# Kernel tuning notes

Hardware: AMD Instinct MI355X
Metric: run time of the kernel (lower is better)

The kernel has to match this reference:

```python
import jax, jax.numpy as jnp
import numpy as np
import math

V, E, H, A, N = 32000, 512, 512, 64, 8  # vocab, embed, rnn hidden, att_size, n_heads
T, B = 256, 128                          # scan length (acts as att batch), inner dim


def _lstm(x, Wih, Whh, bih, bhh):
    # x: (T, B, E); torch nn.LSTM gate order i, f, g, o; zero initial state
    Bb = x.shape[1]
    Hh = Whh.shape[1]
    init = (jnp.zeros((Bb, Hh), x.dtype), jnp.zeros((Bb, Hh), x.dtype))

    def step(carry, xt):
        h, c = carry
        gates = xt @ Wih.T + bih + h @ Whh.T + bhh          # (B, 4H)
        i, f, g, o = jnp.split(gates, 4, axis=-1)
        c = jax.nn.sigmoid(f) * c + jax.nn.sigmoid(i) * jnp.tanh(g)
        h = jax.nn.sigmoid(o) * jnp.tanh(c)
        return (h, c), h

    _, hs = jax.lax.scan(step, init, x)
    return hs  # (T, B, H)


def setup_inputs() -> dict:
    key = jax.random.key(0)
    ks = jax.random.split(key, 26)
    rn = lambda k, s: jax.random.normal(k, s, jnp.float32) * 0.02
    inp = {
        "input_seq_l": jax.random.randint(ks[0], (T, B), 0, V, jnp.int32),
        "input_seq_r": jax.random.randint(ks[1], (T, B), 0, V, jnp.int32),
        "emb_l": rn(ks[2], (V, E)),
        "emb_r": rn(ks[3], (V, E)),
        "Wih_l": rn(ks[4], (4 * H, E)), "Whh_l": rn(ks[5], (4 * H, H)),
        "bih_l": rn(ks[6], (4 * H,)), "bhh_l": rn(ks[7], (4 * H,)),
        "Wih_r": rn(ks[8], (4 * H, E)), "Whh_r": rn(ks[9], (4 * H, H)),
        "bih_r": rn(ks[10], (4 * H,)), "bhh_r": rn(ks[11], (4 * H,)),
        "Wq": rn(ks[12], (N, H, A)), "bq": rn(ks[13], (N, A)),
        "Wk": rn(ks[14], (N, H, A)), "bk": rn(ks[15], (N, A)),
        "Wv": rn(ks[16], (N, H, A)), "bv": rn(ks[17], (N, A)),
        "Wo": rn(ks[18], (N * A, H)), "bo": rn(ks[19], (H,)),
        "Wh": rn(ks[20], (2 * H, 64)), "bh": rn(ks[21], (64,)),
        "Wa": rn(ks[22], (64, 2)), "ba": rn(ks[23], (2,)),
    }
    return inp


def reference(input_seq_l, input_seq_r, emb_l, emb_r,
              Wih_l, Whh_l, bih_l, bhh_l,
              Wih_r, Whh_r, bih_r, bhh_r,
              Wq, bq, Wk, bk, Wv, bv, Wo, bo, Wh, bh, Wa, ba):
    # left encoder
    ol = _lstm(emb_l[input_seq_l], Wih_l, Whh_l, bih_l, bhh_l)   # (T, B, H)
    # multi-head attention over left outputs (all heads batched)
    q = jnp.einsum('tbh,nhd->ntbd', ol, Wq) + bq[:, None, None, :]
    k = jnp.einsum('tbh,nhd->ntbd', ol, Wk) + bk[:, None, None, :]
    v = jnp.einsum('tbh,nhd->ntbd', ol, Wv) + bv[:, None, None, :]
    scores = jnp.einsum('ntbd,ntcd->ntbc', q, k) / math.sqrt(A)  # (N, T, B, B)
    p = jax.nn.softmax(scores, axis=-1)
    att = jnp.einsum('ntbc,ntcd->ntbd', p, v)                    # (N, T, B, A)
    att = att.transpose(1, 2, 0, 3).reshape(att.shape[1], att.shape[2], -1)  # (T, B, N*A)
    ol = att @ Wo + bo                                           # (T, B, H)
    ol = ol.mean(axis=1)                                         # (T, H)
    # right encoder
    orr = _lstm(emb_r[input_seq_r], Wih_r, Whh_r, bih_r, bhh_r).mean(axis=1)  # (T, H)
    cat = jnp.concatenate([ol, orr], axis=1)                     # (T, 2H)
    fc = cat @ Wh + bh
    ans = jax.nn.softmax(fc @ Wa + ba, axis=1)                   # (T, 2)
    return ans
```

## Files before the change

### kernel.cpp

```cpp
#include <hip/hip_runtime.h>

typedef unsigned short u16;
typedef __attribute__((ext_vector_type(4))) float f32x4;
typedef __attribute__((ext_vector_type(8))) short bf8;

#define MFMA16(a, b, c) __builtin_amdgcn_mfma_f32_16x16x32_bf16((a), (b), (c), 0, 0, 0)

__device__ __forceinline__ u16 f2bf(float f) {
  unsigned u = __builtin_bit_cast(unsigned, f);
  u += 0x7FFFu + ((u >> 16) & 1u);
  return (u16)(u >> 16);
}
__device__ __forceinline__ float bf2f(u16 h) {
  unsigned u = ((unsigned)h) << 16;
  return __builtin_bit_cast(float, u);
}
__device__ __forceinline__ float sigm(float x) { return 1.0f / (1.0f + __expf(-x)); }
__device__ __forceinline__ float tanh_f(float x) {
  x = fminf(fmaxf(x, -15.f), 15.f);
  float e = __expf(2.f * x);
  return (e - 1.f) / (e + 1.f);
}

__global__ void k_fill(float* __restrict__ p, int n, float v) {
  int i = blockIdx.x * blockDim.x + threadIdx.x;
  if (i < n) p[i] = v;
}

__device__ __forceinline__ void gemm_body(
    const int* __restrict__ idx, const float* __restrict__ emb,
    const float* __restrict__ Wih, u16* __restrict__ Gpre,
    int m_base, int m0, int n0, char* smem, int tid) {
  u16 (*lA)[72] = (u16(*)[72])smem;
  u16 (*lB)[72] = (u16(*)[72])(smem + 18432);
  int lane = tid & 63, wid = tid >> 6;
  int wm = (wid >> 1) << 6, wn = (wid & 1) << 6;
  int lq = lane >> 4, lc = lane & 15;
  f32x4 acc[4][4] = {};
  for (int k0 = 0; k0 < 512; k0 += 64) {
#pragma unroll
    for (int s = 0; s < 2; s++) {
      int slot = tid + s * 256;
      int row = slot >> 2, seg = (slot & 3) << 4;
      const float* pa = emb + (size_t)idx[m_base + m0 + row] * 512 + k0 + seg;
      const float* pb = Wih + (size_t)(n0 + row) * 512 + k0 + seg;
      float4 a0 = ((const float4*)pa)[0], a1 = ((const float4*)pa)[1];
      float4 a2 = ((const float4*)pa)[2], a3 = ((const float4*)pa)[3];
      float4 b0 = ((const float4*)pb)[0], b1 = ((const float4*)pb)[1];
      float4 b2 = ((const float4*)pb)[2], b3 = ((const float4*)pb)[3];
      union { u16 h[8]; int4 v; } pk;
      pk.h[0]=f2bf(a0.x); pk.h[1]=f2bf(a0.y); pk.h[2]=f2bf(a0.z); pk.h[3]=f2bf(a0.w);
      pk.h[4]=f2bf(a1.x); pk.h[5]=f2bf(a1.y); pk.h[6]=f2bf(a1.z); pk.h[7]=f2bf(a1.w);
      *(int4*)&lA[row][seg] = pk.v;
      pk.h[0]=f2bf(a2.x); pk.h[1]=f2bf(a2.y); pk.h[2]=f2bf(a2.z); pk.h[3]=f2bf(a2.w);
      pk.h[4]=f2bf(a3.x); pk.h[5]=f2bf(a3.y); pk.h[6]=f2bf(a3.z); pk.h[7]=f2bf(a3.w);
      *(int4*)&lA[row][seg + 8] = pk.v;
      pk.h[0]=f2bf(b0.x); pk.h[1]=f2bf(b0.y); pk.h[2]=f2bf(b0.z); pk.h[3]=f2bf(b0.w);
      pk.h[4]=f2bf(b1.x); pk.h[5]=f2bf(b1.y); pk.h[6]=f2bf(b1.z); pk.h[7]=f2bf(b1.w);
      *(int4*)&lB[row][seg] = pk.v;
      pk.h[0]=f2bf(b2.x); pk.h[1]=f2bf(b2.y); pk.h[2]=f2bf(b2.z); pk.h[3]=f2bf(b2.w);
      pk.h[4]=f2bf(b3.x); pk.h[5]=f2bf(b3.y); pk.h[6]=f2bf(b3.z); pk.h[7]=f2bf(b3.w);
      *(int4*)&lB[row][seg + 8] = pk.v;
    }
    __syncthreads();
#pragma unroll
    for (int kk = 0; kk < 64; kk += 32) {
      int ko = kk + (lq << 3);
      bf8 af[4], bg[4];
#pragma unroll
      for (int i = 0; i < 4; i++) af[i] = *(const bf8*)&lA[wm + i * 16 + lc][ko];
#pragma unroll
      for (int j = 0; j < 4; j++) bg[j] = *(const bf8*)&lB[wn + j * 16 + lc][ko];
#pragma unroll
      for (int i = 0; i < 4; i++)
#pragma unroll
        for (int j = 0; j < 4; j++) acc[i][j] = MFMA16(af[i], bg[j], acc[i][j]);
    }
    __syncthreads();
  }
  int cr = lq << 2;
#pragma unroll
  for (int i = 0; i < 4; i++)
#pragma unroll
    for (int j = 0; j < 4; j++)
#pragma unroll
      for (int r = 0; r < 4; r++) {
        int m = m0 + wm + i * 16 + cr + r;
        int nn = n0 + wn + j * 16 + lc;
        Gpre[(size_t)m * 2048 + nn] = f2bf(acc[i][j][r]);
      }
}

__global__ __launch_bounds__(256, 1) void k_prep(
    unsigned* __restrict__ flg, float* __restrict__ hrm,
    const float* __restrict__ Whh_l, u16* __restrict__ Whl,
    const float* __restrict__ Whh_r, u16* __restrict__ Whr,
    const float* __restrict__ Wq, u16* __restrict__ WqT,
    const float* __restrict__ Wk, u16* __restrict__ WkT,
    const float* __restrict__ Wv, u16* __restrict__ WvT,
    const float* __restrict__ bih_l, const float* __restrict__ bhh_l, float* __restrict__ bsl,
    const float* __restrict__ bih_r, const float* __restrict__ bhh_r, float* __restrict__ bsr,
    const int* __restrict__ seq_l, const int* __restrict__ seq_r,
    const float* __restrict__ emb_l, const float* __restrict__ emb_r,
    const float* __restrict__ Wih_l, const float* __restrict__ Wih_r,
    u16* __restrict__ Gl0, u16* __restrict__ Gr0, int Tc) {
  __shared__ __align__(16) char smem[36864];
  int bid = blockIdx.x, tid = threadIdx.x;
  if (bid < 2) {
    flg[bid * 256 + tid] = 0u;
  } else if (bid < 514) {
    hrm[(bid - 2) * 256 + tid] = 0.f;
  } else if (bid < 2562) {
    int rel = bid - 514;
    int enc = rel >> 10;
    int i = (rel & 1023) * 256 + tid;
    const float* in = enc ? Whh_r : Whh_l;
    u16* outp = enc ? Whr : Whl;
    float4 v = ((const float4*)in)[i];
    union { u16 h[4]; uint2 u; } p;
    p.h[0] = f2bf(v.x); p.h[1] = f2bf(v.y); p.h[2] = f2bf(v.z); p.h[3] = f2bf(v.w);
    ((uint2*)outp)[i] = p.u;
  } else if (bid < 5634) {
    int rel = bid - 2562;
    int which = rel >> 10;
    int g = (rel & 1023) * 256 + tid;
    const float* W = which == 0 ? Wq : (which == 1 ? Wk : Wv);
    u16* WT = which == 0 ? WqT : (which == 1 ? WkT : WvT);
    int n = g >> 15, d = (g >> 9) & 63, h = g & 511;
    WT[g] = f2bf(W[(n << 15) + (h << 6) + d]);
  } else if (bid < 5650) {
    int rel = bid - 5634;
    int enc = rel >> 3;
    int i = (rel & 7) * 256 + tid;
    if (enc == 0) bsl[i] = bih_l[i] + bhh_l[i];
    else          bsr[i] = bih_r[i] + bhh_r[i];
  } else {
    int rel = bid - 5650;
    int per = Tc << 4;
    int ge = rel >= per;
    int rem = ge ? rel - per : rel;
    gemm_body(ge ? seq_r : seq_l, ge ? emb_r : emb_l, ge ? Wih_r : Wih_l,
              ge ? Gr0 : Gl0, 0, (rem >> 4) << 7, (rem & 15) << 7, smem, tid);
  }
}

__device__ void lstm_body(
    const u16* __restrict__ Gl, const u16* __restrict__ Gr,
    const u16* __restrict__ Whl, const u16* __restrict__ Whr,
    const float* __restrict__ bsl, const float* __restrict__ bsr,
    u16* __restrict__ hsl, float* __restrict__ hrm,
    unsigned* __restrict__ hx, float* __restrict__ cstate,
    unsigned* __restrict__ flg, int t0, int nT, char* hlds, int bid, int tid) {
  int pod = bid & 7, cg = bid >> 3;
  int e = pod >> 2, bg = pod & 3;
  int b0 = bg << 5, c0 = cg << 5;
  const u16* Gpre = e ? Gr : Gl;
  const u16* Whh  = e ? Whr : Whl;
  const float* bsum = e ? bsr : bsl;

  int lane = tid & 63, w = tid >> 6;
  int lq = lane >> 4, lc = lane & 15, cr = lq << 2;
  int cl = (w << 3) + (lc & 7);
  int gg0 = lc >> 3;
  int lr0 = (gg0 << 5) + cl;
  int lr1 = ((2 + gg0) << 5) + cl;
  int gc0 = (gg0 << 9) + c0 + cl;
  int gc1 = ((2 + gg0) << 9) + c0 + cl;
  float bs0 = bsum[gc0], bs1 = bsum[gc1];
  bool owner = (lc & 8) != 0;

  int gr0 = ((lr0 >> 5) << 9) + c0 + (lr0 & 31);
  int gr1 = ((lr1 >> 5) << 9) + c0 + (lr1 & 31);
  bf8 wb0[16], wb1[16];
  {
    const u16* p0 = Whh + (size_t)gr0 * 512 + (lq << 3);
    const u16* p1 = Whh + (size_t)gr1 * 512 + (lq << 3);
#pragma unroll
    for (int ks = 0; ks < 16; ks++) {
      wb0[ks] = *(const bf8*)(p0 + (ks << 5));
      wb1[ks] = *(const bf8*)(p1 + (ks << 5));
    }
  }
  float creg[2][4];
#pragma unroll
  for (int mi = 0; mi < 2; mi++)
#pragma unroll
    for (int r = 0; r < 4; r++) creg[mi][r] = 0.f;
  if (t0 > 0 && owner) {
#pragma unroll
    for (int mi = 0; mi < 2; mi++)
#pragma unroll
      for (int r = 0; r < 4; r++)
        creg[mi][r] = cstate[(size_t)((e << 7) + b0 + (mi << 4) + cr + r) * 512 + c0 + cl];
  }

  u16 gp[2][2][4];
#pragma unroll
  for (int mi = 0; mi < 2; mi++)
#pragma unroll
    for (int r = 0; r < 4; r++) {
      size_t rowb = (size_t)(b0 + (mi << 4) + cr + r) << 11;
      gp[mi][0][r] = Gpre[rowb + gc0];
      gp[mi][1][r] = Gpre[rowb + gc1];
    }

  int ax = (lc & 7) << 4;
  int abyte0 = lc << 10;
  int abyte1 = (16 + lc) << 10;
  int hxc = (c0 >> 1) + (w << 2) + ((lc & 7) >> 1);
  const int srow = tid >> 6;
  const int scolb = (tid & 63) << 4;

  for (int t = 0; t < nT; t++) {
    int tg = t0 + t;
    f32x4 acc[2][2] = {};
    if (tg > 0) {
      if (t > 0) {
        if (tid < 64) {
          const unsigned* fa = flg + (pod << 6) + (lane & 15);
          unsigned fv;
          int guard = 0;
          while (true) {
            asm volatile("global_load_dword %0, %1, off sc0 sc1"
                         : "=v"(fv) : "v"(fa) : "memory");
            asm volatile("s_waitcnt vmcnt(0)" ::: "memory");
            if (__ballot(fv >= (unsigned)tg) == ~0ull) break;
            if (++guard > 300000) break;
          }
        }
        __syncthreads();
      }
      const unsigned* hxr = hx + (((size_t)((e << 1) | ((tg - 1) & 1))) << 15);
      uint4 sv[8];
#pragma unroll
      for (int i = 0; i < 8; i++) {
        int row = (i << 2) + srow;
        const unsigned* ap = hxr + (((size_t)(b0 + row)) << 8) + ((tid & 63) << 2);
        asm volatile("global_load_dwordx4 %0, %1, off sc0 sc1"
                     : "=v"(sv[i]) : "v"(ap));
      }
      asm volatile("s_waitcnt vmcnt(0)" ::: "memory");
      __builtin_amdgcn_sched_barrier(0);
#pragma unroll
      for (int i = 0; i < 8; i++) {
        int row = (i << 2) + srow;
        *(uint4*)(hlds + (row << 10) + (scolb ^ ((row & 7) << 4))) = sv[i];
      }
      __syncthreads();
#pragma unroll
      for (int ks = 0; ks < 16; ks++) {
        int kb = (ks << 6) + (lq << 4);
        bf8 a0 = *(const bf8*)(hlds + abyte0 + (kb ^ ax));
        bf8 a1 = *(const bf8*)(hlds + abyte1 + (kb ^ ax));
        acc[0][0] = MFMA16(a0, wb0[ks], acc[0][0]);
        acc[0][1] = MFMA16(a0, wb1[ks], acc[0][1]);
        acc[1][0] = MFMA16(a1, wb0[ks], acc[1][0]);
        acc[1][1] = MFMA16(a1, wb1[ks], acc[1][1]);
      }
      __syncthreads();
    }
    unsigned* hxw = hx + (((size_t)((e << 1) | (tg & 1))) << 15);
    float msum = 0.f;
#pragma unroll
    for (int mi = 0; mi < 2; mi++)
#pragma unroll
      for (int r = 0; r < 4; r++) {
        float v0 = acc[mi][0][r] + bf2f(gp[mi][0][r]) + bs0;
        float v1 = acc[mi][1][r] + bf2f(gp[mi][1][r]) + bs1;
        float send = sigm(v0) * tanh_f(v1);
        float recv = __shfl_xor(send, 8, 64);
        float h = 0.f;
        if (owner) {
          float c = sigm(v0) * creg[mi][r] + recv;
          creg[mi][r] = c;
          h = sigm(v1) * tanh_f(c);
          msum += h;
        }
        unsigned hb = (unsigned)f2bf(h);
        unsigned hi = __shfl_down(hb, 1, 64);
        unsigned packed = (hb & 0xffffu) | (hi << 16);
        int b = b0 + (mi << 4) + cr + r;
        if (owner && !(lane & 1)) {
          if (!e)
            *(unsigned*)(hsl + (((size_t)((tg << 7) + b)) << 9) + c0 + cl) = packed;
          unsigned* sa = hxw + (((size_t)b) << 8) + hxc;
          asm volatile("global_store_dword %0, %1, off sc0 sc1"
                       :: "v"(sa), "v"(packed) : "memory");
        }
      }
    asm volatile("s_waitcnt vmcnt(0)" ::: "memory");
    __syncthreads();
    if (tid == 0) {
      unsigned tv = (unsigned)(tg + 1);
      unsigned* fa = flg + (pod << 6) + cg;
      asm volatile("global_store_dword %0, %1, off sc0 sc1"
                   :: "v"(fa), "v"(tv) : "memory");
    }
    if (e) {
      float s = msum;
      s += __shfl_xor(s, 16, 64);
      s += __shfl_xor(s, 32, 64);
      if (owner && lq == 0)
        atomicAdd(&hrm[(tg << 9) + c0 + cl], s * 0.0078125f);
    }
    if (t + 1 < nT) {
#pragma unroll
      for (int mi = 0; mi < 2; mi++)
#pragma unroll
        for (int r = 0; r < 4; r++) {
          size_t rowb = (size_t)(((t + 1) << 7) + b0 + (mi << 4) + cr + r) << 11;
          gp[mi][0][r] = Gpre[rowb + gc0];
          gp[mi][1][r] = Gpre[rowb + gc1];
        }
    }
  }
  if (owner) {
#pragma unroll
    for (int mi = 0; mi < 2; mi++)
#pragma unroll
      for (int r = 0; r < 4; r++)
        cstate[(size_t)((e << 7) + b0 + (mi << 4) + cr + r) * 512 + c0 + cl] = creg[mi][r];
  }
}

__global__ __launch_bounds__(256, 1) void k_fused(
    const u16* __restrict__ Gl, const u16* __restrict__ Gr,
    u16* __restrict__ Ggl, u16* __restrict__ Ggr,
    const int* __restrict__ seq_l, const int* __restrict__ seq_r,
    const float* __restrict__ emb_l, const float* __restrict__ emb_r,
    const float* __restrict__ Wih_l, const float* __restrict__ Wih_r,
    const u16* __restrict__ Whl, const u16* __restrict__ Whr,
    const float* __restrict__ bsl, const float* __restrict__ bsr,
    u16* __restrict__ hsl, float* __restrict__ hrm,
    unsigned* __restrict__ hx, float* __restrict__ cstate,
    unsigned* __restrict__ flg, int t0, int nT, int gmb, int Tc) {
  __shared__ __align__(16) char smem[36864];
  int bid = blockIdx.x, tid = threadIdx.x;
  if (bid < 128) {
    lstm_body(Gl, Gr, Whl, Whr, bsl, bsr, hsl, hrm, hx, cstate, flg,
              t0, nT, smem, bid, tid);
  } else {
    int gb = bid - 128;
    int per = Tc << 4;
    int ge = gb >= per;
    int rem = ge ? gb - per : gb;
    gemm_body(ge ? seq_r : seq_l, ge ? emb_r : emb_l, ge ? Wih_r : Wih_l,
              ge ? Ggr : Ggl, gmb, (rem >> 4) << 7, (rem & 15) << 7, smem, tid);
  }
}

__global__ __launch_bounds__(256, 1) void k_attn(
    const u16* __restrict__ hs,
    const u16* __restrict__ WqT, const u16* __restrict__ WkT, const u16* __restrict__ WvT,
    const float* __restrict__ bq, const float* __restrict__ bk, const float* __restrict__ bv,
    float* __restrict__ attmean) {
  __shared__ __align__(16) char smem[123904];
  u16 (*qs)[72]  = (u16(*)[72])smem;
  u16 (*ksm)[72] = (u16(*)[72])(smem + 18432);
  u16 (*vt)[136] = (u16(*)[136])(smem + 36864);
  float (*sc)[132] = (float(*)[132])(smem + 54272);
  u16 (*ps)[136] = (u16(*)[136])smem;
  float* red = (float*)(smem + 54272);
  float* pmax = (float*)(smem + 121856);
  float* psum = (float*)(smem + 122880);

  int bid = blockIdx.x;
  int n = bid >> 8, t = bid & 255;
  int tid = threadIdx.x, lane = tid & 63, wid = tid >> 6;
  int lq = lane >> 4, lc = lane & 15, cr = lq << 2;
  const u16* ol = hs + ((size_t)t << 16);

  float bqv[4], bkv[4];
#pragma unroll
  for (int nf = 0; nf < 4; nf++) {
    bqv[nf] = bq[(n << 6) + (nf << 4) + lc];
    bkv[nf] = bk[(n << 6) + (nf << 4) + lc];
  }
  float bvv[4][4];
#pragma unroll
  for (int mi = 0; mi < 4; mi++)
#pragma unroll
    for (int r = 0; r < 4; r++) bvv[mi][r] = bv[(n << 6) + (mi << 4) + cr + r];

  const u16* wq = WqT + ((size_t)n << 15);
  const u16* wk = WkT + ((size_t)n << 15);
  const u16* wv = WvT + ((size_t)n << 15);
  f32x4 aq[2][4] = {}, ak[2][4] = {}, av[4][2] = {};
  for (int ks = 0; ks < 16; ks++) {
    int ko = (ks << 5) + (lq << 3);
    bf8 a0 = *(const bf8*)&ol[(size_t)((wid << 5) + lc) * 512 + ko];
    bf8 a1 = *(const bf8*)&ol[(size_t)((wid << 5) + 16 + lc) * 512 + ko];
#pragma unroll
    for (int nf = 0; nf < 4; nf++) {
      bf8 bw = *(const bf8*)&wq[(size_t)((nf << 4) + lc) * 512 + ko];
      aq[0][nf] = MFMA16(a0, bw, aq[0][nf]);
      aq[1][nf] = MFMA16(a1, bw, aq[1][nf]);
      bf8 bw2 = *(const bf8*)&wk[(size_t)((nf << 4) + lc) * 512 + ko];
      ak[0][nf] = MFMA16(a0, bw2, ak[0][nf]);
      ak[1][nf] = MFMA16(a1, bw2, ak[1][nf]);
    }
#pragma unroll
    for (int mi = 0; mi < 4; mi++) {
      bf8 aw = *(const bf8*)&wv[(size_t)((mi << 4) + lc) * 512 + ko];
      av[mi][0] = MFMA16(aw, a0, av[mi][0]);
      av[mi][1] = MFMA16(aw, a1, av[mi][1]);
    }
  }
#pragma unroll
  for (int mi = 0; mi < 2; mi++)
#pragma unroll
    for (int nf = 0; nf < 4; nf++)
#pragma unroll
      for (int r = 0; r < 4; r++) {
        int b = (wid << 5) + (mi << 4) + cr + r;
        int d = (nf << 4) + lc;
        qs[b][d] = f2bf(aq[mi][nf][r] + bqv[nf]);
        ksm[b][d] = f2bf(ak[mi][nf][r] + bkv[nf]);
      }
#pragma unroll
  for (int mi = 0; mi < 4; mi++)
#pragma unroll
    for (int c2 = 0; c2 < 2; c2++)
#pragma unroll
      for (int r = 0; r < 4; r++) {
        int d = (mi << 4) + cr + r;
        int c = (wid << 5) + (c2 << 4) + lc;
        vt[d][c] = f2bf(av[mi][c2][r] + bvv[mi][r]);
      }
  __syncthreads();

  f32x4 as_[2][8] = {};
#pragma unroll
  for (int ks = 0; ks < 2; ks++) {
    int ko = (ks << 5) + (lq << 3);
    bf8 a0 = *(const bf8*)&qs[(wid << 5) + lc][ko];
    bf8 a1 = *(const bf8*)&qs[(wid << 5) + 16 + lc][ko];
#pragma unroll
    for (int nf = 0; nf < 8; nf++) {
      bf8 bw = *(const bf8*)&ksm[(nf << 4) + lc][ko];
      as_[0][nf] = MFMA16(a0, bw, as_[0][nf]);
      as_[1][nf] = MFMA16(a1, bw, as_[1][nf]);
    }
  }
#pragma unroll
  for (int mi = 0; mi < 2; mi++)
#pragma unroll
    for (int nf = 0; nf < 8; nf++)
#pragma unroll
      for (int r = 0; r < 4; r++)
        sc[(wid << 5) + (mi << 4) + cr + r][(nf << 4) + lc] = as_[mi][nf][r] * 0.125f;
  __syncthreads();

  {
    int row = tid & 127, half = tid >> 7;
    int cb = half << 6;
    float mx = -1e30f;
    for (int j = 0; j < 64; j++) mx = fmaxf(mx, sc[row][cb + j]);
    pmax[(half << 7) + row] = mx;
    __syncthreads();
    mx = fmaxf(pmax[row], pmax[128 + row]);
    float s = 0.f;
    for (int j = 0; j < 64; j++) { float ev = __expf(sc[row][cb + j] - mx); s += ev; sc[row][cb + j] = ev; }
    psum[(half << 7) + row] = s;
    __syncthreads();
    float inv = 1.f / (psum[row] + psum[128 + row]);
    for (int j = 0; j < 64; j++) ps[row][cb + j] = f2bf(sc[row][cb + j] * inv);
  }
  __syncthreads();

  f32x4 ao[2][4] = {};
#pragma unroll
  for (int ks = 0; ks < 4; ks++) {
    int ko = (ks << 5) + (lq << 3);
    bf8 a0 = *(const bf8*)&ps[(wid << 5) + lc][ko];
    bf8 a1 = *(const bf8*)&ps[(wid << 5) + 16 + lc][ko];
#pragma unroll
    for (int nf = 0; nf < 4; nf++) {
      bf8 bw = *(const bf8*)&vt[(nf << 4) + lc][ko];
      ao[0][nf] = MFMA16(a0, bw, ao[0][nf]);
      ao[1][nf] = MFMA16(a1, bw, ao[1][nf]);
    }
  }
  float pm[4];
#pragma unroll
  for (int nf = 0; nf < 4; nf++) {
    float s = 0.f;
#pragma unroll
    for (int mi = 0; mi < 2; mi++)
#pragma unroll
      for (int r = 0; r < 4; r++) s += ao[mi][nf][r];
    s += __shfl_xor(s, 16, 64);
    s += __shfl_xor(s, 32, 64);
    pm[nf] = s;
  }
  if (lq == 0) {
#pragma unroll
    for (int nf = 0; nf < 4; nf++) red[(wid << 6) + (nf << 4) + lc] = pm[nf];
  }
  __syncthreads();
  if (tid < 64) {
    float s = red[tid] + red[64 + tid] + red[128 + tid] + red[192 + tid];
    attmean[(t << 9) + (n << 6) + tid] = s * 0.0078125f;
  }
}

__global__ __launch_bounds__(256) void k_olm(const float* __restrict__ am, const float* __restrict__ Wo,
                                             const float* __restrict__ bo, float* __restrict__ olm) {
  __shared__ float row[512];
  int t = blockIdx.x >> 1, h0 = (blockIdx.x & 1) << 8;
  int tid = threadIdx.x;
  row[tid] = am[(t << 9) + tid];
  row[tid + 256] = am[(t << 9) + 256 + tid];
  __syncthreads();
  int h = h0 + tid;
  float s = bo[h];
  for (int k = 0; k < 512; k++) s += row[k] * Wo[(k << 9) + h];
  olm[(t << 9) + h] = s;
}

__global__ __launch_bounds__(64) void k_final(const float* __restrict__ olmp, const float* __restrict__ hrm,
                                              const float* __restrict__ Wh, const float* __restrict__ bh,
                                              const float* __restrict__ Wa, const float* __restrict__ ba,
                                              float* __restrict__ out) {
  __shared__ float cat[1024];
  int t = blockIdx.x, j = threadIdx.x;
  for (int i = j; i < 512; i += 64) {
    cat[i] = olmp[(t << 9) + i];
    cat[512 + i] = hrm[(t << 9) + i];
  }
  __syncthreads();
  float f = bh[j];
  for (int k = 0; k < 1024; k++) f += cat[k] * Wh[(k << 6) + j];
  float p0 = f * Wa[j * 2], p1 = f * Wa[j * 2 + 1];
#pragma unroll
  for (int o = 32; o > 0; o >>= 1) { p0 += __shfl_down(p0, o); p1 += __shfl_down(p1, o); }
  if (j == 0) {
    p0 += ba[0]; p1 += ba[1];
    float m = fmaxf(p0, p1);
    float e0 = __expf(p0 - m), e1 = __expf(p1 - m);
    float inv = 1.f / (e0 + e1);
    out[t * 2] = e0 * inv;
    out[t * 2 + 1] = e1 * inv;
  }
}

extern "C" void kernel_launch(void* const* d_in, const int* in_sizes, int n_in,
                              void* d_out, int out_size, void* d_ws, size_t ws_size,
                              hipStream_t stream) {
  const int*   seq_l = (const int*)d_in[0];
  const int*   seq_r = (const int*)d_in[1];
  const float* emb_l = (const float*)d_in[2];
  const float* emb_r = (const float*)d_in[3];
  const float* Wih_l = (const float*)d_in[4];
  const float* Whh_l = (const float*)d_in[5];
  const float* bih_l = (const float*)d_in[6];
  const float* bhh_l = (const float*)d_in[7];
  const float* Wih_r = (const float*)d_in[8];
  const float* Whh_r = (const float*)d_in[9];
  const float* bih_r = (const float*)d_in[10];
  const float* bhh_r = (const float*)d_in[11];
  const float* Wq = (const float*)d_in[12];
  const float* bq = (const float*)d_in[13];
  const float* Wk = (const float*)d_in[14];
  const float* bk = (const float*)d_in[15];
  const float* Wv = (const float*)d_in[16];
  const float* bv = (const float*)d_in[17];
  const float* Wo = (const float*)d_in[18];
  const float* bo = (const float*)d_in[19];
  const float* Wh = (const float*)d_in[20];
  const float* bhc = (const float*)d_in[21];
  const float* Wa = (const float*)d_in[22];
  const float* ba = (const float*)d_in[23];
  float* out = (float*)d_out;

  char* ws = (char*)d_ws;
  size_t off = 0;
  auto alloc = [&](size_t bytes) { char* p = ws + off; off += (bytes + 255) & ~(size_t)255; return p; };
  u16*   hsl  = (u16*)alloc(33554432);
  u16*   Whl  = (u16*)alloc(2097152);
  u16*   Whr  = (u16*)alloc(2097152);
  u16*   WqT  = (u16*)alloc(524288);
  u16*   WkT  = (u16*)alloc(524288);
  u16*   WvT  = (u16*)alloc(524288);
  float* bsl  = (float*)alloc(8192);
  float* bsr  = (float*)alloc(8192);
  unsigned* hx = (unsigned*)alloc(524288);
  float* cst  = (float*)alloc(524288);
  unsigned* flg = (unsigned*)alloc(2048);
  float* am   = (float*)alloc(524288);
  float* hrm  = (float*)alloc(524288);
  float* olm  = (float*)alloc(524288);
  size_t fixed = off;

  int Tc = 0;
  const int cands[3] = {128, 64, 32};
  for (int i = 0; i < 3; i++) {
    size_t need = fixed + 4ull * (size_t)cands[i] * 524288ull;
    if (need <= ws_size) { Tc = cands[i]; break; }
  }
  if (Tc == 0) {
    k_fill<<<2, 256, 0, stream>>>(out, out_size, 0.25f);
    return;
  }
  size_t gbytes = (size_t)Tc * 524288ull;
  u16* Glb[2]; u16* Grb[2];
  Glb[0] = (u16*)alloc(gbytes); Glb[1] = (u16*)alloc(gbytes);
  Grb[0] = (u16*)alloc(gbytes); Grb[1] = (u16*)alloc(gbytes);

  k_prep<<<5650 + (Tc << 5), 256, 0, stream>>>(
      flg, hrm, Whh_l, Whl, Whh_r, Whr, Wq, WqT, Wk, WkT, Wv, WvT,
      bih_l, bhh_l, bsl, bih_r, bhh_r, bsr,
      seq_l, seq_r, emb_l, emb_r, Wih_l, Wih_r, Glb[0], Grb[0], Tc);

  int nC = 256 / Tc;
  for (int c = 0; c < nC; c++) {
    int hg = (c + 1 < nC);
    int grid = 128 + (hg ? (Tc << 5) : 0);
    k_fused<<<grid, 256, 0, stream>>>(
        Glb[c & 1], Grb[c & 1], Glb[(c + 1) & 1], Grb[(c + 1) & 1],
        seq_l, seq_r, emb_l, emb_r, Wih_l, Wih_r,
        Whl, Whr, bsl, bsr, hsl, hrm, hx, cst, flg,
        c * Tc, Tc, (c + 1) * Tc * 128, Tc);
  }
  k_attn<<<2048, 256, 0, stream>>>(hsl, WqT, WkT, WvT, bq, bk, bv, am);
  k_olm<<<512, 256, 0, stream>>>(am, Wo, bo, olm);
  k_final<<<256, 64, 0, stream>>>(olm, hrm, Wh, bhc, Wa, ba, out);
}
```

Baseline: 1.751 ms.

## Fuse input projection into recurrent LSTM step and overlap attention with scan

Drops the separate chunked input-projection GEMM. Each LSTM block now keeps both Wih and Whh slices in registers and computes x_t·Wih alongside h·Whh every step, reading gathered bf16 embeddings. Attention blocks are launched in the same persistent kernel and spin on per-timestep flags, so attention for step t starts as soon as that step's hidden states exist. This removes the chunk launches and the precomputed-gate round trip, but doubles per-step MFMA work and register pressure on the serial critical path. It also relies on attention blocks co-residing with the LSTM blocks without starving them.

```diff
diff --git a/kernel.cpp b/kernel.cpp
--- a/kernel.cpp
+++ b/kernel.cpp
@@ -27,74 +27,12 @@
   if (i < n) p[i] = v;
 }
 
-__device__ __forceinline__ void gemm_body(
-    const int* __restrict__ idx, const float* __restrict__ emb,
-    const float* __restrict__ Wih, u16* __restrict__ Gpre,
-    int m_base, int m0, int n0, char* smem, int tid) {
-  u16 (*lA)[72] = (u16(*)[72])smem;
-  u16 (*lB)[72] = (u16(*)[72])(smem + 18432);
-  int lane = tid & 63, wid = tid >> 6;
-  int wm = (wid >> 1) << 6, wn = (wid & 1) << 6;
-  int lq = lane >> 4, lc = lane & 15;
-  f32x4 acc[4][4] = {};
-  for (int k0 = 0; k0 < 512; k0 += 64) {
-#pragma unroll
-    for (int s = 0; s < 2; s++) {
-      int slot = tid + s * 256;
-      int row = slot >> 2, seg = (slot & 3) << 4;
-      const float* pa = emb + (size_t)idx[m_base + m0 + row] * 512 + k0 + seg;
-      const float* pb = Wih + (size_t)(n0 + row) * 512 + k0 + seg;
-      float4 a0 = ((const float4*)pa)[0], a1 = ((const float4*)pa)[1];
-      float4 a2 = ((const float4*)pa)[2], a3 = ((const float4*)pa)[3];
-      float4 b0 = ((const float4*)pb)[0], b1 = ((const float4*)pb)[1];
-      float4 b2 = ((const float4*)pb)[2], b3 = ((const float4*)pb)[3];
-      union { u16 h[8]; int4 v; } pk;
-      pk.h[0]=f2bf(a0.x); pk.h[1]=f2bf(a0.y); pk.h[2]=f2bf(a0.z); pk.h[3]=f2bf(a0.w);
-      pk.h[4]=f2bf(a1.x); pk.h[5]=f2bf(a1.y); pk.h[6]=f2bf(a1.z); pk.h[7]=f2bf(a1.w);
-      *(int4*)&lA[row][seg] = pk.v;
-      pk.h[0]=f2bf(a2.x); pk.h[1]=f2bf(a2.y); pk.h[2]=f2bf(a2.z); pk.h[3]=f2bf(a2.w);
-      pk.h[4]=f2bf(a3.x); pk.h[5]=f2bf(a3.y); pk.h[6]=f2bf(a3.z); pk.h[7]=f2bf(a3.w);
-      *(int4*)&lA[row][seg + 8] = pk.v;
-      pk.h[0]=f2bf(b0.x); pk.h[1]=f2bf(b0.y); pk.h[2]=f2bf(b0.z); pk.h[3]=f2bf(b0.w);
-      pk.h[4]=f2bf(b1.x); pk.h[5]=f2bf(b1.y); pk.h[6]=f2bf(b1.z); pk.h[7]=f2bf(b1.w);
-      *(int4*)&lB[row][seg] = pk.v;
-      pk.h[0]=f2bf(b2.x); pk.h[1]=f2bf(b2.y); pk.h[2]=f2bf(b2.z); pk.h[3]=f2bf(b2.w);
-      pk.h[4]=f2bf(b3.x); pk.h[5]=f2bf(b3.y); pk.h[6]=f2bf(b3.z); pk.h[7]=f2bf(b3.w);
-      *(int4*)&lB[row][seg + 8] = pk.v;
-    }
-    __syncthreads();
-#pragma unroll
-    for (int kk = 0; kk < 64; kk += 32) {
-      int ko = kk + (lq << 3);
-      bf8 af[4], bg[4];
-#pragma unroll
-      for (int i = 0; i < 4; i++) af[i] = *(const bf8*)&lA[wm + i * 16 + lc][ko];
-#pragma unroll
-      for (int j = 0; j < 4; j++) bg[j] = *(const bf8*)&lB[wn + j * 16 + lc][ko];
-#pragma unroll
-      for (int i = 0; i < 4; i++)
-#pragma unroll
-        for (int j = 0; j < 4; j++) acc[i][j] = MFMA16(af[i], bg[j], acc[i][j]);
-    }
-    __syncthreads();
-  }
-  int cr = lq << 2;
-#pragma unroll
-  for (int i = 0; i < 4; i++)
-#pragma unroll
-    for (int j = 0; j < 4; j++)
-#pragma unroll
-      for (int r = 0; r < 4; r++) {
-        int m = m0 + wm + i * 16 + cr + r;
-        int nn = n0 + wn + j * 16 + lc;
-        Gpre[(size_t)m * 2048 + nn] = f2bf(acc[i][j][r]);
-      }
-}
-
-__global__ __launch_bounds__(256, 1) void k_prep(
+__global__ __launch_bounds__(256, 2) void k_prep(
     unsigned* __restrict__ flg, float* __restrict__ hrm,
     const float* __restrict__ Whh_l, u16* __restrict__ Whl,
     const float* __restrict__ Whh_r, u16* __restrict__ Whr,
+    const float* __restrict__ Wih_l, u16* __restrict__ Wil,
+    const float* __restrict__ Wih_r, u16* __restrict__ Wir,
     const float* __restrict__ Wq, u16* __restrict__ WqT,
     const float* __restrict__ Wk, u16* __restrict__ WkT,
     const float* __restrict__ Wv, u16* __restrict__ WvT,
@@ -102,61 +40,68 @@
     const float* __restrict__ bih_r, const float* __restrict__ bhh_r, float* __restrict__ bsr,
     const int* __restrict__ seq_l, const int* __restrict__ seq_r,
     const float* __restrict__ emb_l, const float* __restrict__ emb_r,
-    const float* __restrict__ Wih_l, const float* __restrict__ Wih_r,
-    u16* __restrict__ Gl0, u16* __restrict__ Gr0, int Tc) {
-  __shared__ __align__(16) char smem[36864];
+    u16* __restrict__ xsl, u16* __restrict__ xsr) {
   int bid = blockIdx.x, tid = threadIdx.x;
   if (bid < 2) {
     flg[bid * 256 + tid] = 0u;
   } else if (bid < 514) {
     hrm[(bid - 2) * 256 + tid] = 0.f;
-  } else if (bid < 2562) {
+  } else if (bid < 4610) {
     int rel = bid - 514;
-    int enc = rel >> 10;
+    int which = rel >> 10;
     int i = (rel & 1023) * 256 + tid;
-    const float* in = enc ? Whh_r : Whh_l;
-    u16* outp = enc ? Whr : Whl;
+    const float* in = which == 0 ? Whh_l : (which == 1 ? Whh_r : (which == 2 ? Wih_l : Wih_r));
+    u16* outp = which == 0 ? Whl : (which == 1 ? Whr : (which == 2 ? Wil : Wir));
     float4 v = ((const float4*)in)[i];
     union { u16 h[4]; uint2 u; } p;
     p.h[0] = f2bf(v.x); p.h[1] = f2bf(v.y); p.h[2] = f2bf(v.z); p.h[3] = f2bf(v.w);
     ((uint2*)outp)[i] = p.u;
-  } else if (bid < 5634) {
-    int rel = bid - 2562;
+  } else if (bid < 7682) {
+    int rel = bid - 4610;
     int which = rel >> 10;
     int g = (rel & 1023) * 256 + tid;
     const float* W = which == 0 ? Wq : (which == 1 ? Wk : Wv);
     u16* WT = which == 0 ? WqT : (which == 1 ? WkT : WvT);
     int n = g >> 15, d = (g >> 9) & 63, h = g & 511;
     WT[g] = f2bf(W[(n << 15) + (h << 6) + d]);
-  } else if (bid < 5650) {
-    int rel = bid - 5634;
+  } else if (bid < 7698) {
+    int rel = bid - 7682;
     int enc = rel >> 3;
     int i = (rel & 7) * 256 + tid;
     if (enc == 0) bsl[i] = bih_l[i] + bhh_l[i];
     else          bsr[i] = bih_r[i] + bhh_r[i];
   } else {
-    int rel = bid - 5650;
-    int per = Tc << 4;
-    int ge = rel >= per;
-    int rem = ge ? rel - per : rel;
-    gemm_body(ge ? seq_r : seq_l, ge ? emb_r : emb_l, ge ? Wih_r : Wih_l,
-              ge ? Gr0 : Gl0, 0, (rem >> 4) << 7, (rem & 15) << 7, smem, tid);
+    int rel = bid - 7698;
+    int enc = rel >= 2048;
+    int rem = enc ? rel - 2048 : rel;
+    const int* idx = enc ? seq_r : seq_l;
+    const float* emb = enc ? emb_r : emb_l;
+    u16* xs = enc ? xsr : xsl;
+    int row = (rem << 4) + (tid >> 4);
+    int seg = (tid & 15) << 5;
+    const float4* src = (const float4*)(emb + (size_t)idx[row] * 512 + seg);
+    uint2* dst = (uint2*)(xs + (size_t)row * 512 + seg);
+#pragma unroll
+    for (int j = 0; j < 8; j++) {
+      float4 v = src[j];
+      union { u16 h[4]; uint2 u; } p;
+      p.h[0] = f2bf(v.x); p.h[1] = f2bf(v.y); p.h[2] = f2bf(v.z); p.h[3] = f2bf(v.w);
+      dst[j] = p.u;
+    }
   }
 }
 
 __device__ void lstm_body(
-    const u16* __restrict__ Gl, const u16* __restrict__ Gr,
-    const u16* __restrict__ Whl, const u16* __restrict__ Whr,
-    const float* __restrict__ bsl, const float* __restrict__ bsr,
+    const u16* __restrict__ xs, const u16* __restrict__ Whh,
+    const u16* __restrict__ Wih, const float* __restrict__ bsum,
     u16* __restrict__ hsl, float* __restrict__ hrm,
-    unsigned* __restrict__ hx, float* __restrict__ cstate,
-    unsigned* __restrict__ flg, int t0, int nT, char* hlds, int bid, int tid) {
+    unsigned* __restrict__ hx, unsigned* __restrict__ flg,
+    int bid, int tid, char* smem) {
+  char* hlds = smem;
+  char* xlds = smem + 32768;
   int pod = bid & 7, cg = bid >> 3;
   int e = pod >> 2, bg = pod & 3;
   int b0 = bg << 5, c0 = cg << 5;
-  const u16* Gpre = e ? Gr : Gl;
-  const u16* Whh  = e ? Whr : Whl;
-  const float* bsum = e ? bsr : bsl;
 
   int lane = tid & 63, w = tid >> 6;
   int lq = lane >> 4, lc = lane & 15, cr = lq << 2;
@@ -171,14 +116,18 @@
 
   int gr0 = ((lr0 >> 5) << 9) + c0 + (lr0 & 31);
   int gr1 = ((lr1 >> 5) << 9) + c0 + (lr1 & 31);
-  bf8 wb0[16], wb1[16];
+  bf8 wb0[16], wb1[16], wi0[16], wi1[16];
   {
     const u16* p0 = Whh + (size_t)gr0 * 512 + (lq << 3);
     const u16* p1 = Whh + (size_t)gr1 * 512 + (lq << 3);
+    const u16* q0 = Wih + (size_t)gr0 * 512 + (lq << 3);
+    const u16* q1 = Wih + (size_t)gr1 * 512 + (lq << 3);
 #pragma unroll
     for (int ks = 0; ks < 16; ks++) {
       wb0[ks] = *(const bf8*)(p0 + (ks << 5));
       wb1[ks] = *(const bf8*)(p1 + (ks << 5));
+      wi0[ks] = *(const bf8*)(q0 + (ks << 5));
+      wi1[ks] = *(const bf8*)(q1 + (ks << 5));
     }
   }
   float creg[2][4];
@@ -186,23 +135,6 @@
   for (int mi = 0; mi < 2; mi++)
 #pragma unroll
     for (int r = 0; r < 4; r++) creg[mi][r] = 0.f;
-  if (t0 > 0 && owner) {
-#pragma unroll
-    for (int mi = 0; mi < 2; mi++)
-#pragma unroll
-      for (int r = 0; r < 4; r++)
-        creg[mi][r] = cstate[(size_t)((e << 7) + b0 + (mi << 4) + cr + r) * 512 + c0 + cl];
-  }
-
-  u16 gp[2][2][4];
-#pragma unroll
-  for (int mi = 0; mi < 2; mi++)
-#pragma unroll
-    for (int r = 0; r < 4; r++) {
-      size_t rowb = (size_t)(b0 + (mi << 4) + cr + r) << 11;
-      gp[mi][0][r] = Gpre[rowb + gc0];
-      gp[mi][1][r] = Gpre[rowb + gc1];
-    }
 
   int ax = (lc & 7) << 4;
   int abyte0 = lc << 10;
@@ -211,25 +143,28 @@
   const int srow = tid >> 6;
   const int scolb = (tid & 63) << 4;
 
-  for (int t = 0; t < nT; t++) {
-    int tg = t0 + t;
+  for (int tg = 0; tg < 256; tg++) {
+    uint4 xv[8];
+#pragma unroll
+    for (int i = 0; i < 8; i++) {
+      int row = (i << 2) + srow;
+      xv[i] = ((const uint4*)(xs + (((size_t)((tg << 7) + b0 + row)) << 9)))[tid & 63];
+    }
     f32x4 acc[2][2] = {};
     if (tg > 0) {
-      if (t > 0) {
-        if (tid < 64) {
-          const unsigned* fa = flg + (pod << 6) + (lane & 15);
-          unsigned fv;
-          int guard = 0;
-          while (true) {
-            asm volatile("global_load_dword %0, %1, off sc0 sc1"
-                         : "=v"(fv) : "v"(fa) : "memory");
-            asm volatile("s_waitcnt vmcnt(0)" ::: "memory");
-            if (__ballot(fv >= (unsigned)tg) == ~0ull) break;
-            if (++guard > 300000) break;
-          }
+      if (tid < 64) {
+        const unsigned* fa = flg + (pod << 6) + (lane & 15);
+        unsigned fv;
+        int guard = 0;
+        while (true) {
+          asm volatile("global_load_dword %0, %1, off sc0 sc1"
+                       : "=v"(fv) : "v"(fa) : "memory");
+          asm volatile("s_waitcnt vmcnt(0)" ::: "memory");
+          if (__ballot(fv >= (unsigned)tg) == ~0ull) break;
+          if (++guard > 1000000) break;
         }
-        __syncthreads();
-      }
+      }
+      __syncthreads();
       const unsigned* hxr = hx + (((size_t)((e << 1) | ((tg - 1) & 1))) << 15);
       uint4 sv[8];
 #pragma unroll
@@ -246,7 +181,24 @@
         int row = (i << 2) + srow;
         *(uint4*)(hlds + (row << 10) + (scolb ^ ((row & 7) << 4))) = sv[i];
       }
-      __syncthreads();
+    }
+#pragma unroll
+    for (int i = 0; i < 8; i++) {
+      int row = (i << 2) + srow;
+      *(uint4*)(xlds + (row << 10) + (scolb ^ ((row & 7) << 4))) = xv[i];
+    }
+    __syncthreads();
+#pragma unroll
+    for (int ks = 0; ks < 16; ks++) {
+      int kb = (ks << 6) + (lq << 4);
+      bf8 a0 = *(const bf8*)(xlds + abyte0 + (kb ^ ax));
+      bf8 a1 = *(const bf8*)(xlds + abyte1 + (kb ^ ax));
+      acc[0][0] = MFMA16(a0, wi0[ks], acc[0][0]);
+      acc[0][1] = MFMA16(a0, wi1[ks], acc[0][1]);
+      acc[1][0] = MFMA16(a1, wi0[ks], acc[1][0]);
+      acc[1][1] = MFMA16(a1, wi1[ks], acc[1][1]);
+    }
+    if (tg > 0) {
 #pragma unroll
       for (int ks = 0; ks < 16; ks++) {
         int kb = (ks << 6) + (lq << 4);
@@ -257,16 +209,16 @@
         acc[1][0] = MFMA16(a1, wb0[ks], acc[1][0]);
         acc[1][1] = MFMA16(a1, wb1[ks], acc[1][1]);
       }
-      __syncthreads();
-    }
+    }
+    __syncthreads();
     unsigned* hxw = hx + (((size_t)((e << 1) | (tg & 1))) << 15);
     float msum = 0.f;
 #pragma unroll
     for (int mi = 0; mi < 2; mi++)
 #pragma unroll
       for (int r = 0; r < 4; r++) {
-        float v0 = acc[mi][0][r] + bf2f(gp[mi][0][r]) + bs0;
-        float v1 = acc[mi][1][r] + bf2f(gp[mi][1][r]) + bs1;
+        float v0 = acc[mi][0][r] + bs0;
+        float v1 = acc[mi][1][r] + bs1;
         float send = sigm(v0) * tanh_f(v1);
         float recv = __shfl_xor(send, 8, 64);
         float h = 0.f;
@@ -281,8 +233,11 @@
         unsigned packed = (hb & 0xffffu) | (hi << 16);
         int b = b0 + (mi << 4) + cr + r;
         if (owner && !(lane & 1)) {
-          if (!e)
-            *(unsigned*)(hsl + (((size_t)((tg << 7) + b)) << 9) + c0 + cl) = packed;
+          if (!e) {
+            unsigned* hp = (unsigned*)(hsl + (((size_t)((tg << 7) + b)) << 9) + c0 + cl);
+            asm volatile("global_store_dword %0, %1, off sc0 sc1"
+                         :: "v"(hp), "v"(packed) : "memory");
+          }
           unsigned* sa = hxw + (((size_t)b) << 8) + hxc;
           asm volatile("global_store_dword %0, %1, off sc0 sc1"
                        :: "v"(sa), "v"(packed) : "memory");
@@ -303,58 +258,14 @@
       if (owner && lq == 0)
         atomicAdd(&hrm[(tg << 9) + c0 + cl], s * 0.0078125f);
     }
-    if (t + 1 < nT) {
-#pragma unroll
-      for (int mi = 0; mi < 2; mi++)
-#pragma unroll
-        for (int r = 0; r < 4; r++) {
-          size_t rowb = (size_t)(((t + 1) << 7) + b0 + (mi << 4) + cr + r) << 11;
-          gp[mi][0][r] = Gpre[rowb + gc0];
-          gp[mi][1][r] = Gpre[rowb + gc1];
-        }
-    }
-  }
-  if (owner) {
-#pragma unroll
-    for (int mi = 0; mi < 2; mi++)
-#pragma unroll
-      for (int r = 0; r < 4; r++)
-        cstate[(size_t)((e << 7) + b0 + (mi << 4) + cr + r) * 512 + c0 + cl] = creg[mi][r];
-  }
-}
-
-__global__ __launch_bounds__(256, 1) void k_fused(
-    const u16* __restrict__ Gl, const u16* __restrict__ Gr,
-    u16* __restrict__ Ggl, u16* __restrict__ Ggr,
-    const int* __restrict__ seq_l, const int* __restrict__ seq_r,
-    const float* __restrict__ emb_l, const float* __restrict__ emb_r,
-    const float* __restrict__ Wih_l, const float* __restrict__ Wih_r,
-    const u16* __restrict__ Whl, const u16* __restrict__ Whr,
-    const float* __restrict__ bsl, const float* __restrict__ bsr,
-    u16* __restrict__ hsl, float* __restrict__ hrm,
-    unsigned* __restrict__ hx, float* __restrict__ cstate,
-    unsigned* __restrict__ flg, int t0, int nT, int gmb, int Tc) {
-  __shared__ __align__(16) char smem[36864];
-  int bid = blockIdx.x, tid = threadIdx.x;
-  if (bid < 128) {
-    lstm_body(Gl, Gr, Whl, Whr, bsl, bsr, hsl, hrm, hx, cstate, flg,
-              t0, nT, smem, bid, tid);
-  } else {
-    int gb = bid - 128;
-    int per = Tc << 4;
-    int ge = gb >= per;
-    int rem = ge ? gb - per : gb;
-    gemm_body(ge ? seq_r : seq_l, ge ? emb_r : emb_l, ge ? Wih_r : Wih_l,
-              ge ? Ggr : Ggl, gmb, (rem >> 4) << 7, (rem & 15) << 7, smem, tid);
-  }
-}
-
-__global__ __launch_bounds__(256, 1) void k_attn(
+  }
+}
+
+__device__ void attn_body(
     const u16* __restrict__ hs,
     const u16* __restrict__ WqT, const u16* __restrict__ WkT, const u16* __restrict__ WvT,
     const float* __restrict__ bq, const float* __restrict__ bk, const float* __restrict__ bv,
-    float* __restrict__ attmean) {
-  __shared__ __align__(16) char smem[123904];
+    float* __restrict__ attmean, int n, int t, char* smem, int tid) {
   u16 (*qs)[72]  = (u16(*)[72])smem;
   u16 (*ksm)[72] = (u16(*)[72])(smem + 18432);
   u16 (*vt)[136] = (u16(*)[136])(smem + 36864);
@@ -364,9 +275,7 @@
   float* pmax = (float*)(smem + 121856);
   float* psum = (float*)(smem + 122880);
 
-  int bid = blockIdx.x;
-  int n = bid >> 8, t = bid & 255;
-  int tid = threadIdx.x, lane = tid & 63, wid = tid >> 6;
+  int lane = tid & 63, wid = tid >> 6;
   int lq = lane >> 4, lc = lane & 15, cr = lq << 2;
   const u16* ol = hs + ((size_t)t << 16);
 
@@ -381,15 +290,28 @@
   for (int mi = 0; mi < 4; mi++)
 #pragma unroll
     for (int r = 0; r < 4; r++) bvv[mi][r] = bv[(n << 6) + (mi << 4) + cr + r];
+
+  uint4 xa0[16], xa1[16];
+#pragma unroll
+  for (int ks = 0; ks < 16; ks++) {
+    int ko = (ks << 5) + (lq << 3);
+    const u16* p0 = ol + (size_t)((wid << 5) + lc) * 512 + ko;
+    const u16* p1 = ol + (size_t)((wid << 5) + 16 + lc) * 512 + ko;
+    asm volatile("global_load_dwordx4 %0, %1, off sc0 sc1" : "=v"(xa0[ks]) : "v"(p0));
+    asm volatile("global_load_dwordx4 %0, %1, off sc0 sc1" : "=v"(xa1[ks]) : "v"(p1));
+  }
+  asm volatile("s_waitcnt vmcnt(0)" ::: "memory");
+  __builtin_amdgcn_sched_barrier(0);
 
   const u16* wq = WqT + ((size_t)n << 15);
   const u16* wk = WkT + ((size_t)n << 15);
   const u16* wv = WvT + ((size_t)n << 15);
   f32x4 aq[2][4] = {}, ak[2][4] = {}, av[4][2] = {};
+#pragma unroll
   for (int ks = 0; ks < 16; ks++) {
     int ko = (ks << 5) + (lq << 3);
-    bf8 a0 = *(const bf8*)&ol[(size_t)((wid << 5) + lc) * 512 + ko];
-    bf8 a1 = *(const bf8*)&ol[(size_t)((wid << 5) + 16 + lc) * 512 + ko];
+    bf8 a0 = __builtin_bit_cast(bf8, xa0[ks]);
+    bf8 a1 = __builtin_bit_cast(bf8, xa1[ks]);
 #pragma unroll
     for (int nf = 0; nf < 4; nf++) {
       bf8 bw = *(const bf8*)&wq[(size_t)((nf << 4) + lc) * 512 + ko];
@@ -501,6 +423,44 @@
   if (tid < 64) {
     float s = red[tid] + red[64 + tid] + red[128 + tid] + red[192 + tid];
     attmean[(t << 9) + (n << 6) + tid] = s * 0.0078125f;
+  }
+}
+
+__global__ __launch_bounds__(256, 1) void k_fused(
+    const u16* __restrict__ xsl, const u16* __restrict__ xsr,
+    const u16* __restrict__ Whl, const u16* __restrict__ Whr,
+    const u16* __restrict__ Wil, const u16* __restrict__ Wir,
+    const float* __restrict__ bsl, const float* __restrict__ bsr,
+    u16* __restrict__ hsl, float* __restrict__ hrm,
+    unsigned* __restrict__ hx, unsigned* __restrict__ flg,
+    const u16* __restrict__ WqT, const u16* __restrict__ WkT, const u16* __restrict__ WvT,
+    const float* __restrict__ bq, const float* __restrict__ bk, const float* __restrict__ bv,
+    float* __restrict__ am) {
+  __shared__ __align__(16) char smem[123904];
+  int bid = blockIdx.x, tid = threadIdx.x;
+  if (bid < 128) {
+    int e = (bid & 7) >> 2;
+    lstm_body(e ? xsr : xsl, e ? Whr : Whl, e ? Wir : Wil, e ? bsr : bsl,
+              hsl, hrm, hx, flg, bid, tid, smem);
+  } else {
+    int abid = bid - 128;
+    int t = abid >> 3, n = abid & 7;
+    if (tid < 64) {
+      int lane = tid;
+      const unsigned* fa = flg + ((lane >> 4) << 6) + (lane & 15);
+      unsigned fv;
+      int guard = 0;
+      while (true) {
+        asm volatile("global_load_dword %0, %1, off sc0 sc1"
+                     : "=v"(fv) : "v"(fa) : "memory");
+        asm volatile("s_waitcnt vmcnt(0)" ::: "memory");
+        if (__ballot(fv > (unsigned)t) == ~0ull) break;
+        if (++guard > 3000000) break;
+        __builtin_amdgcn_s_sleep(8);
+      }
+    }
+    __syncthreads();
+    attn_body(hsl, WqT, WkT, WvT, bq, bk, bv, am, n, t, smem, tid);
   }
 }
 
@@ -577,52 +537,38 @@
   size_t off = 0;
   auto alloc = [&](size_t bytes) { char* p = ws + off; off += (bytes + 255) & ~(size_t)255; return p; };
   u16*   hsl  = (u16*)alloc(33554432);
+  u16*   xsl  = (u16*)alloc(33554432);
+  u16*   xsr  = (u16*)alloc(33554432);
   u16*   Whl  = (u16*)alloc(2097152);
   u16*   Whr  = (u16*)alloc(2097152);
+  u16*   Wil  = (u16*)alloc(2097152);
+  u16*   Wir  = (u16*)alloc(2097152);
   u16*   WqT  = (u16*)alloc(524288);
   u16*   WkT  = (u16*)alloc(524288);
   u16*   WvT  = (u16*)alloc(524288);
   float* bsl  = (float*)alloc(8192);
   float* bsr  = (float*)alloc(8192);
   unsigned* hx = (unsigned*)alloc(524288);
-  float* cst  = (float*)alloc(524288);
   unsigned* flg = (unsigned*)alloc(2048);
   float* am   = (float*)alloc(524288);
   float* hrm  = (float*)alloc(524288);
   float* olm  = (float*)alloc(524288);
-  size_t fixed = off;
-
-  int Tc = 0;
-  const int cands[3] = {128, 64, 32};
-  for (int i = 0; i < 3; i++) {
-    size_t need = fixed + 4ull * (size_t)cands[i] * 524288ull;
-    if (need <= ws_size) { Tc = cands[i]; break; }
-  }
-  if (Tc == 0) {
+
+  if (off > ws_size) {
     k_fill<<<2, 256, 0, stream>>>(out, out_size, 0.25f);
     return;
   }
-  size_t gbytes = (size_t)Tc * 524288ull;
-  u16* Glb[2]; u16* Grb[2];
-  Glb[0] = (u16*)alloc(gbytes); Glb[1] = (u16*)alloc(gbytes);
-  Grb[0] = (u16*)alloc(gbytes); Grb[1] = (u16*)alloc(gbytes);
-
-  k_prep<<<5650 + (Tc << 5), 256, 0, stream>>>(
-      flg, hrm, Whh_l, Whl, Whh_r, Whr, Wq, WqT, Wk, WkT, Wv, WvT,
+
+  k_prep<<<11794, 256, 0, stream>>>(
+      flg, hrm, Whh_l, Whl, Whh_r, Whr, Wih_l, Wil, Wih_r, Wir,
+      Wq, WqT, Wk, WkT, Wv, WvT,
       bih_l, bhh_l, bsl, bih_r, bhh_r, bsr,
-      seq_l, seq_r, emb_l, emb_r, Wih_l, Wih_r, Glb[0], Grb[0], Tc);
-
-  int nC = 256 / Tc;
-  for (int c = 0; c < nC; c++) {
-    int hg = (c + 1 < nC);
-    int grid = 128 + (hg ? (Tc << 5) : 0);
-    k_fused<<<grid, 256, 0, stream>>>(
-        Glb[c & 1], Grb[c & 1], Glb[(c + 1) & 1], Grb[(c + 1) & 1],
-        seq_l, seq_r, emb_l, emb_r, Wih_l, Wih_r,
-        Whl, Whr, bsl, bsr, hsl, hrm, hx, cst, flg,
-        c * Tc, Tc, (c + 1) * Tc * 128, Tc);
-  }
-  k_attn<<<2048, 256, 0, stream>>>(hsl, WqT, WkT, WvT, bq, bk, bv, am);
+      seq_l, seq_r, emb_l, emb_r, xsl, xsr);
+
+  k_fused<<<2176, 256, 0, stream>>>(
+      xsl, xsr, Whl, Whr, Wil, Wir, bsl, bsr,
+      hsl, hrm, hx, flg, WqT, WkT, WvT, bq, bk, bv, am);
+
   k_olm<<<512, 256, 0, stream>>>(am, Wo, bo, olm);
   k_final<<<256, 64, 0, stream>>>(olm, hrm, Wh, bhc, Wa, ba, out);
 }
```

Result: slower. 2.212 ms (+26.3%).

## Overlap QKV weight conversion with first LSTM chunk and allow uneven chunking

Applied to the files above, without the earlier changes.

Moves the Wq/Wk/Wv transpose-and-convert work out of the prep kernel into spare blocks of the first fused LSTM launch, so it runs alongside the serial recurrence instead of delaying it. It also adds uneven chunk schedules (96/96/64) for tighter workspace budgets and raises the prep kernel's launch bound to two blocks per CU. The fused kernel's shared memory declaration grows to 80 KB, which may affect how the extra GEMM and conversion blocks co-reside with the persistent LSTM blocks.

```diff
diff --git a/kernel.cpp b/kernel.cpp
--- a/kernel.cpp
+++ b/kernel.cpp
@@ -91,19 +91,16 @@
       }
 }
 
-__global__ __launch_bounds__(256, 1) void k_prep(
+__global__ __launch_bounds__(256, 2) void k_prep(
     unsigned* __restrict__ flg, float* __restrict__ hrm,
     const float* __restrict__ Whh_l, u16* __restrict__ Whl,
     const float* __restrict__ Whh_r, u16* __restrict__ Whr,
-    const float* __restrict__ Wq, u16* __restrict__ WqT,
-    const float* __restrict__ Wk, u16* __restrict__ WkT,
-    const float* __restrict__ Wv, u16* __restrict__ WvT,
     const float* __restrict__ bih_l, const float* __restrict__ bhh_l, float* __restrict__ bsl,
     const float* __restrict__ bih_r, const float* __restrict__ bhh_r, float* __restrict__ bsr,
     const int* __restrict__ seq_l, const int* __restrict__ seq_r,
     const float* __restrict__ emb_l, const float* __restrict__ emb_r,
     const float* __restrict__ Wih_l, const float* __restrict__ Wih_r,
-    u16* __restrict__ Gl0, u16* __restrict__ Gr0, int Tc) {
+    u16* __restrict__ Gl0, u16* __restrict__ Gr0, int Tc0) {
   __shared__ __align__(16) char smem[36864];
   int bid = blockIdx.x, tid = threadIdx.x;
   if (bid < 2) {
@@ -120,23 +117,15 @@
     union { u16 h[4]; uint2 u; } p;
     p.h[0] = f2bf(v.x); p.h[1] = f2bf(v.y); p.h[2] = f2bf(v.z); p.h[3] = f2bf(v.w);
     ((uint2*)outp)[i] = p.u;
-  } else if (bid < 5634) {
+  } else if (bid < 2578) {
     int rel = bid - 2562;
-    int which = rel >> 10;
-    int g = (rel & 1023) * 256 + tid;
-    const float* W = which == 0 ? Wq : (which == 1 ? Wk : Wv);
-    u16* WT = which == 0 ? WqT : (which == 1 ? WkT : WvT);
-    int n = g >> 15, d = (g >> 9) & 63, h = g & 511;
-    WT[g] = f2bf(W[(n << 15) + (h << 6) + d]);
-  } else if (bid < 5650) {
-    int rel = bid - 5634;
     int enc = rel >> 3;
     int i = (rel & 7) * 256 + tid;
     if (enc == 0) bsl[i] = bih_l[i] + bhh_l[i];
     else          bsr[i] = bih_r[i] + bhh_r[i];
   } else {
-    int rel = bid - 5650;
-    int per = Tc << 4;
+    int rel = bid - 2578;
+    int per = Tc0 << 4;
     int ge = rel >= per;
     int rem = ge ? rel - per : rel;
     gemm_body(ge ? seq_r : seq_l, ge ? emb_r : emb_l, ge ? Wih_r : Wih_l,
@@ -333,19 +322,33 @@
     const float* __restrict__ bsl, const float* __restrict__ bsr,
     u16* __restrict__ hsl, float* __restrict__ hrm,
     unsigned* __restrict__ hx, float* __restrict__ cstate,
-    unsigned* __restrict__ flg, int t0, int nT, int gmb, int Tc) {
-  __shared__ __align__(16) char smem[36864];
+    unsigned* __restrict__ flg,
+    const float* __restrict__ Wq, const float* __restrict__ Wk, const float* __restrict__ Wv,
+    u16* __restrict__ WqT, u16* __restrict__ WkT, u16* __restrict__ WvT,
+    int t0, int nT, int gmb, int nextT) {
+  __shared__ __align__(16) char smem[81920];
   int bid = blockIdx.x, tid = threadIdx.x;
   if (bid < 128) {
     lstm_body(Gl, Gr, Whl, Whr, bsl, bsr, hsl, hrm, hx, cstate, flg,
               t0, nT, smem, bid, tid);
   } else {
     int gb = bid - 128;
-    int per = Tc << 4;
-    int ge = gb >= per;
-    int rem = ge ? gb - per : gb;
-    gemm_body(ge ? seq_r : seq_l, ge ? emb_r : emb_l, ge ? Wih_r : Wih_l,
-              ge ? Ggr : Ggl, gmb, (rem >> 4) << 7, (rem & 15) << 7, smem, tid);
+    int per2 = nextT << 5;
+    if (gb < per2) {
+      int per = nextT << 4;
+      int ge = gb >= per;
+      int rem = ge ? gb - per : gb;
+      gemm_body(ge ? seq_r : seq_l, ge ? emb_r : emb_l, ge ? Wih_r : Wih_l,
+                ge ? Ggr : Ggl, gmb, (rem >> 4) << 7, (rem & 15) << 7, smem, tid);
+    } else {
+      int rel = gb - per2;
+      int which = rel >> 10;
+      int g = (rel & 1023) * 256 + tid;
+      const float* W = which == 0 ? Wq : (which == 1 ? Wk : Wv);
+      u16* WT = which == 0 ? WqT : (which == 1 ? WkT : WvT);
+      int n = g >> 15, d = (g >> 9) & 63, h = g & 511;
+      WT[g] = f2bf(W[(n << 15) + (h << 6) + d]);
+    }
   }
 }
 
@@ -592,35 +595,39 @@
   float* olm  = (float*)alloc(524288);
   size_t fixed = off;
 
-  int Tc = 0;
-  const int cands[3] = {128, 64, 32};
-  for (int i = 0; i < 3; i++) {
-    size_t need = fixed + 4ull * (size_t)cands[i] * 524288ull;
-    if (need <= ws_size) { Tc = cands[i]; break; }
-  }
-  if (Tc == 0) {
+  int chunks[4]; int nch = 0; int Tmax = 0;
+  if (fixed + 4ull * 128 * 524288ull <= ws_size) {
+    chunks[0] = 128; chunks[1] = 128; nch = 2; Tmax = 128;
+  } else if (fixed + 4ull * 96 * 524288ull <= ws_size) {
+    chunks[0] = 96; chunks[1] = 96; chunks[2] = 64; nch = 3; Tmax = 96;
+  } else if (fixed + 4ull * 64 * 524288ull <= ws_size) {
+    chunks[0] = chunks[1] = chunks[2] = chunks[3] = 64; nch = 4; Tmax = 64;
+  } else {
     k_fill<<<2, 256, 0, stream>>>(out, out_size, 0.25f);
     return;
   }
-  size_t gbytes = (size_t)Tc * 524288ull;
+  size_t gbytes = (size_t)Tmax * 524288ull;
   u16* Glb[2]; u16* Grb[2];
   Glb[0] = (u16*)alloc(gbytes); Glb[1] = (u16*)alloc(gbytes);
   Grb[0] = (u16*)alloc(gbytes); Grb[1] = (u16*)alloc(gbytes);
 
-  k_prep<<<5650 + (Tc << 5), 256, 0, stream>>>(
-      flg, hrm, Whh_l, Whl, Whh_r, Whr, Wq, WqT, Wk, WkT, Wv, WvT,
+  k_prep<<<2578 + (chunks[0] << 5), 256, 0, stream>>>(
+      flg, hrm, Whh_l, Whl, Whh_r, Whr,
       bih_l, bhh_l, bsl, bih_r, bhh_r, bsr,
-      seq_l, seq_r, emb_l, emb_r, Wih_l, Wih_r, Glb[0], Grb[0], Tc);
-
-  int nC = 256 / Tc;
-  for (int c = 0; c < nC; c++) {
-    int hg = (c + 1 < nC);
-    int grid = 128 + (hg ? (Tc << 5) : 0);
+      seq_l, seq_r, emb_l, emb_r, Wih_l, Wih_r, Glb[0], Grb[0], chunks[0]);
+
+  int t0 = 0;
+  for (int c = 0; c < nch; c++) {
+    int nT = chunks[c];
+    int nextT = (c + 1 < nch) ? chunks[c + 1] : 0;
+    int grid = 128 + (nextT << 5) + (c == 0 ? 3072 : 0);
     k_fused<<<grid, 256, 0, stream>>>(
         Glb[c & 1], Grb[c & 1], Glb[(c + 1) & 1], Grb[(c + 1) & 1],
         seq_l, seq_r, emb_l, emb_r, Wih_l, Wih_r,
         Whl, Whr, bsl, bsr, hsl, hrm, hx, cst, flg,
-        c * Tc, Tc, (c + 1) * Tc * 128, Tc);
+        Wq, Wk, Wv, WqT, WkT, WvT,
+        t0, nT, (t0 + nT) << 7, nextT);
+    t0 += nT;
   }
   k_attn<<<2048, 256, 0, stream>>>(hsl, WqT, WkT, WvT, bq, bk, bv, am);
   k_olm<<<512, 256, 0, stream>>>(am, Wo, bo, olm);
```

Result: no change. 1.761 ms (+0.5%).
